# Optimization experiments

Hardware: AMD Instinct MI355X
Metric: run time of the kernel (lower is better)

## Reference

```python
import jax, jax.numpy as jnp
import numpy as np

NUM_USERS = 100000
NUM_ITEMS = 50000
N_NODES = NUM_USERS + NUM_ITEMS
N_EDGES = 2400000
EMB = 64
BATCH = 4096
GCN_LAYERS = 3
TAU = 0.2
SSL_LAMBDA = 0.1
REG_LAMBDA = 1e-4


def setup_inputs() -> dict:
    key = jax.random.key(0)
    ks = jax.random.split(key, 8)
    user = jax.random.randint(ks[0], (BATCH,), 0, NUM_USERS, dtype=jnp.int32)
    pos_item = jax.random.randint(ks[1], (BATCH,), 0, NUM_ITEMS, dtype=jnp.int32)
    neg_item = jax.random.randint(ks[2], (BATCH,), 0, NUM_ITEMS, dtype=jnp.int32)
    # symmetric bipartite edges: user -> item and item -> user
    half = N_EDGES // 2
    src_u = jax.random.randint(ks[3], (half,), 0, NUM_USERS, dtype=jnp.int32)
    dst_i = jax.random.randint(ks[4], (half,), NUM_USERS, N_NODES, dtype=jnp.int32)
    adj_row = jnp.concatenate([src_u, dst_i])
    adj_col = jnp.concatenate([dst_i, src_u])
    # normalized-adjacency-like small positive values
    adj_val = jax.random.uniform(ks[5], (N_EDGES,), dtype=jnp.float32) * 0.01
    user_emb_w = jax.random.normal(ks[6], (NUM_USERS, EMB), dtype=jnp.float32) * 0.1
    item_emb_w = jax.random.normal(ks[7], (NUM_ITEMS, EMB), dtype=jnp.float32) * 0.1
    return {"user": user, "pos_item": pos_item, "neg_item": neg_item,
            "adj_row": adj_row, "adj_col": adj_col, "adj_val": adj_val,
            "user_emb_w": user_emb_w, "item_emb_w": item_emb_w}


def _aggregate(adj_row, adj_col, adj_val, user_emb_w, item_emb_w):
    emb = jnp.concatenate([user_emb_w, item_emb_w], axis=0)  # [N, d]
    acc = emb
    e = emb
    for _ in range(GCN_LAYERS):
        # sparse.mm(adj, e): gather columns, scale, scatter-add into rows
        e = jax.ops.segment_sum(adj_val[:, None] * e[adj_col], adj_row,
                                num_segments=N_NODES)
        acc = acc + e
    final = acc / (GCN_LAYERS + 1)  # mean over stacked layer outputs
    return final[:NUM_USERS], final[NUM_USERS:]


def reference(user, pos_item, neg_item, adj_row, adj_col, adj_val,
              user_emb_w, item_emb_w):
    user_all, item_all = _aggregate(adj_row, adj_col, adj_val,
                                    user_emb_w, item_emb_w)
    u = user_all[user]          # [B, d]
    pos = item_all[pos_item]    # [B, d]
    neg = item_all[neg_item]    # [B, d]
    # BPR loss
    pos_s = jnp.sum(u * pos, axis=-1)
    neg_s = jnp.sum(u * neg, axis=-1)
    bpr_loss = -jnp.mean(jax.nn.log_sigmoid(pos_s - neg_s))
    # L2 regularization
    b = u.shape[0]
    reg_loss = 0.5 * (jnp.sum(u * u) + jnp.sum(pos * pos) + jnp.sum(neg * neg)) / b
    reg_loss = reg_loss * REG_LAMBDA
    # neighbor-aggregate SSL (InfoNCE between user and its positive item)
    un = u / jnp.linalg.norm(u, axis=-1, keepdims=True)
    pn = pos / jnp.linalg.norm(pos, axis=-1, keepdims=True)
    logits = un @ pn.T / TAU                       # [B, B]
    pos_logit = jnp.diagonal(logits)
    na_loss = jnp.mean(jax.nn.logsumexp(logits, axis=1) - pos_logit) * SSL_LAMBDA
    return bpr_loss + reg_loss + na_loss
```

## Files before the change

kernel.cpp:

```cpp
#include <hip/hip_runtime.h>
#include <hip/hip_fp16.h>
#include <math.h>

#define NUM_USERS 100000
#define NUM_ITEMS 50000
#define N_NODES   150000
#define N_EDGES   2400000
#define HALF_E    (N_EDGES / 2)
#define EMB       64
#define BATCH     4096
#define TAU        0.2f
#define SSL_LAMBDA 0.1f
#define REG_LAMBDA 1e-4f

#define NB        293
#define BROWS     512
#define CAP       13632
#define BINA_BLK  1024
#define CAST_BLK  9375

__device__ __forceinline__ float wave_sum(float v) {
    #pragma unroll
    for (int m = 1; m < 64; m <<= 1) v += __shfl_xor(v, m, 64);
    return v;
}
__device__ __forceinline__ __half2 bits2h2(int b) {
    union { int i; __half2 h; } u; u.i = b; return u.h;
}
__device__ __forceinline__ int h22bits(__half2 h) {
    union { int i; __half2 h; } u; u.h = h; return u.i;
}
__device__ __forceinline__ float h2f(unsigned short s) {
    union { unsigned short s; __half h; } u; u.s = s; return __half2float(u.h);
}

__global__ __launch_bounds__(256) void prep_kernel(
        const float4* __restrict__ uw4, const float4* __restrict__ iw4,
        uint2* __restrict__ h,
        const int* __restrict__ row, const int* __restrict__ col,
        const float* __restrict__ val,
        int* __restrict__ bucket_cursor, int2* __restrict__ arena) {
    __shared__ int hist[NB];
    const int t = threadIdx.x;
    size_t i = (size_t)blockIdx.x * 256 + t;
    const size_t tot = (size_t)N_NODES * EMB / 4;
    if (i < tot) {
        const size_t nu = (size_t)NUM_USERS * EMB / 4;
        float4 v = (i < nu) ? uw4[i] : iw4[i - nu];
        h[i] = make_uint2(h22bits(__floats2half2_rn(v.x, v.y)),
                          h22bits(__floats2half2_rn(v.z, v.w)));
    }
    if (blockIdx.x >= BINA_BLK) return;
    for (int k = t; k < NB; k += 256) hist[k] = 0;
    __syncthreads();
    const int per = (HALF_E + BINA_BLK - 1) / BINA_BLK;
    const int beg = blockIdx.x * per;
    const int end = min(beg + per, HALF_E);
    for (int e = beg + t; e < end; e += 256) {
        int r = row[e], c = col[e];
        atomicAdd(&hist[r >> 9], 1);
        atomicAdd(&hist[c >> 9], 1);
    }
    __syncthreads();
    for (int k = t; k < NB; k += 256) {
        int cnt = hist[k];
        int base = cnt ? atomicAdd(&bucket_cursor[k], cnt) : 0;
        hist[k] = k * CAP + base;
    }
    __syncthreads();
    for (int e = beg + t; e < end; e += 256) {
        int r = row[e], c = col[e];
        float v1 = val[e], v2 = val[e + HALF_E];
        int s1 = atomicAdd(&hist[r >> 9], 1);
        int s2 = atomicAdd(&hist[c >> 9], 1);
        arena[s1] = make_int2(c | ((r & 511) << 18), __float_as_int(v1));
        arena[s2] = make_int2(r | ((c & 511) << 18), __float_as_int(v2));
    }
}

__global__ __launch_bounds__(256) void bucket_scan(
        const int* __restrict__ bucket_cursor, int* __restrict__ bucket_base,
        int* __restrict__ rowptr) {
    __shared__ int sm[256];
    const int t = threadIdx.x;
    const int K = (NB + 255) / 256;
    int v[K], s = 0;
    #pragma unroll
    for (int j = 0; j < K; j++) {
        int idx = t * K + j;
        v[j] = (idx < NB) ? bucket_cursor[idx] : 0;
        s += v[j];
    }
    sm[t] = s;
    __syncthreads();
    for (int m = 1; m < 256; m <<= 1) {
        int y = (t >= m) ? sm[t - m] : 0;
        __syncthreads();
        sm[t] += y;
        __syncthreads();
    }
    int excl = sm[t] - s;
    #pragma unroll
    for (int j = 0; j < K; j++) {
        int idx = t * K + j;
        if (idx < NB) bucket_base[idx] = excl;
        excl += v[j];
    }
    if (t == 0) rowptr[N_NODES] = N_EDGES;
}

__global__ __launch_bounds__(1024) void bin_sort(
        const int* __restrict__ bucket_cursor, const int* __restrict__ bucket_base,
        const int2* __restrict__ arena,
        int* __restrict__ rowptr, int2* __restrict__ colval) {
    __shared__ int rcnt[BROWS];
    __shared__ int sm[256];
    const int bin = blockIdx.x;
    const int t = threadIdx.x;
    const int total = bucket_cursor[bin];
    const int count = min(total, CAP);
    const int gbase = bucket_base[bin];
    if (t < BROWS) rcnt[t] = 0;
    __syncthreads();
    for (int i = t; i < count; i += 1024) {
        int rx = arena[bin * CAP + i].x >> 18;
        atomicAdd(&rcnt[rx], 1);
    }
    __syncthreads();
    int v0 = 0, v1 = 0, s = 0;
    if (t < 256) {
        v0 = rcnt[2 * t]; v1 = rcnt[2 * t + 1];
        s = v0 + v1;
        sm[t] = s;
    }
    __syncthreads();
    for (int m = 1; m < 256; m <<= 1) {
        int y = (t < 256 && t >= m) ? sm[t - m] : 0;
        __syncthreads();
        if (t < 256) sm[t] += y;
        __syncthreads();
    }
    if (t < 256) {
        int excl = sm[t] - s;
        rcnt[2 * t] = excl;
        rcnt[2 * t + 1] = excl + v0;
        int r0 = bin * BROWS + 2 * t;
        if (r0 < N_NODES) rowptr[r0] = gbase + excl;
        if (r0 + 1 < N_NODES) rowptr[r0 + 1] = gbase + excl + v0;
    }
    __syncthreads();
    for (int i = t; i < count; i += 1024) {
        int2 rec = arena[bin * CAP + i];
        int pos = atomicAdd(&rcnt[rec.x >> 18], 1);
        __half2 hv = __float2half2_rn(__int_as_float(rec.y));
        colval[gbase + pos] = make_int2(rec.x & 0x3FFFF, h22bits(hv));
    }
    for (int i = count + t; i < total; i += 1024)
        colval[gbase + i] = make_int2(0, 0);
}

__global__ __launch_bounds__(256) void spmm_csr(
        const int* __restrict__ rowptr, const int2* __restrict__ colval,
        const unsigned short* __restrict__ h_cur, unsigned short* __restrict__ h_next) {
    const int t = threadIdx.x;
    const int lane = t & 63;
    const int g = lane >> 3;
    const int l = lane & 7;
    int r = blockIdx.x * 4 + (t >> 6);
    if (r >= N_NODES) return;
    const int beg = rowptr[r], end = rowptr[r + 1];
    __half2 ac0 = __float2half2_rn(0.0f), ac1 = ac0, ac2 = ac0, ac3 = ac0;
    int e = beg + g;
    if (e < end) {
        int2 cv = colval[e];
        uint4 x = ((const uint4*)(h_cur + (size_t)cv.x * EMB))[l];
        e += 8;
        if (e < end) {
            int2 cv2 = colval[e];
            uint4 x2 = ((const uint4*)(h_cur + (size_t)cv2.x * EMB))[l];
            for (e += 8; e < end; e += 8) {
                int2 cv3 = colval[e];
                uint4 x3 = ((const uint4*)(h_cur + (size_t)cv3.x * EMB))[l];
                __half2 vv = bits2h2(cv.y);
                ac0 = __hfma2(vv, bits2h2(x.x), ac0);
                ac1 = __hfma2(vv, bits2h2(x.y), ac1);
                ac2 = __hfma2(vv, bits2h2(x.z), ac2);
                ac3 = __hfma2(vv, bits2h2(x.w), ac3);
                cv = cv2; x = x2; cv2 = cv3; x2 = x3;
            }
            __half2 vv = bits2h2(cv.y);
            ac0 = __hfma2(vv, bits2h2(x.x), ac0);
            ac1 = __hfma2(vv, bits2h2(x.y), ac1);
            ac2 = __hfma2(vv, bits2h2(x.z), ac2);
            ac3 = __hfma2(vv, bits2h2(x.w), ac3);
            cv = cv2; x = x2;
        }
        __half2 vv = bits2h2(cv.y);
        ac0 = __hfma2(vv, bits2h2(x.x), ac0);
        ac1 = __hfma2(vv, bits2h2(x.y), ac1);
        ac2 = __hfma2(vv, bits2h2(x.z), ac2);
        ac3 = __hfma2(vv, bits2h2(x.w), ac3);
    }
    int a0 = h22bits(ac0), a1 = h22bits(ac1), a2 = h22bits(ac2), a3 = h22bits(ac3);
    #pragma unroll
    for (int m = 8; m < 64; m <<= 1) {
        a0 = h22bits(__hadd2(bits2h2(a0), bits2h2(__shfl_xor(a0, m, 64))));
        a1 = h22bits(__hadd2(bits2h2(a1), bits2h2(__shfl_xor(a1, m, 64))));
        a2 = h22bits(__hadd2(bits2h2(a2), bits2h2(__shfl_xor(a2, m, 64))));
        a3 = h22bits(__hadd2(bits2h2(a3), bits2h2(__shfl_xor(a3, m, 64))));
    }
    if (g == 0)
        ((uint4*)(h_next + (size_t)r * EMB))[l] =
            make_uint4((unsigned)a0, (unsigned)a1, (unsigned)a2, (unsigned)a3);
}

__global__ __launch_bounds__(256) void spmm_sel(
        const int* __restrict__ rowptr, const int2* __restrict__ colval,
        const int* __restrict__ user, const int* __restrict__ pos,
        const int* __restrict__ neg,
        const unsigned short* __restrict__ h_cur, float* __restrict__ sel) {
    const int t = threadIdx.x;
    const int lane = t & 63;
    const int g = lane >> 3;
    const int l = lane & 7;
    int b = blockIdx.x * 4 + (t >> 6);
    if (b >= 3 * BATCH) return;
    int which = b / BATCH, bb = b - which * BATCH;
    int r = (which == 0) ? user[bb]
          : NUM_USERS + ((which == 1) ? pos[bb] : neg[bb]);
    const int beg = rowptr[r], end = rowptr[r + 1];
    __half2 ac0 = __float2half2_rn(0.0f), ac1 = ac0, ac2 = ac0, ac3 = ac0;
    int e = beg + g;
    if (e < end) {
        int2 cv = colval[e];
        uint4 x = ((const uint4*)(h_cur + (size_t)cv.x * EMB))[l];
        e += 8;
        if (e < end) {
            int2 cv2 = colval[e];
            uint4 x2 = ((const uint4*)(h_cur + (size_t)cv2.x * EMB))[l];
            for (e += 8; e < end; e += 8) {
                int2 cv3 = colval[e];
                uint4 x3 = ((const uint4*)(h_cur + (size_t)cv3.x * EMB))[l];
                __half2 vv = bits2h2(cv.y);
                ac0 = __hfma2(vv, bits2h2(x.x), ac0);
                ac1 = __hfma2(vv, bits2h2(x.y), ac1);
                ac2 = __hfma2(vv, bits2h2(x.z), ac2);
                ac3 = __hfma2(vv, bits2h2(x.w), ac3);
                cv = cv2; x = x2; cv2 = cv3; x2 = x3;
            }
            __half2 vv = bits2h2(cv.y);
            ac0 = __hfma2(vv, bits2h2(x.x), ac0);
            ac1 = __hfma2(vv, bits2h2(x.y), ac1);
            ac2 = __hfma2(vv, bits2h2(x.z), ac2);
            ac3 = __hfma2(vv, bits2h2(x.w), ac3);
            cv = cv2; x = x2;
        }
        __half2 vv = bits2h2(cv.y);
        ac0 = __hfma2(vv, bits2h2(x.x), ac0);
        ac1 = __hfma2(vv, bits2h2(x.y), ac1);
        ac2 = __hfma2(vv, bits2h2(x.z), ac2);
        ac3 = __hfma2(vv, bits2h2(x.w), ac3);
    }
    int a0 = h22bits(ac0), a1 = h22bits(ac1), a2 = h22bits(ac2), a3 = h22bits(ac3);
    #pragma unroll
    for (int m = 8; m < 64; m <<= 1) {
        a0 = h22bits(__hadd2(bits2h2(a0), bits2h2(__shfl_xor(a0, m, 64))));
        a1 = h22bits(__hadd2(bits2h2(a1), bits2h2(__shfl_xor(a1, m, 64))));
        a2 = h22bits(__hadd2(bits2h2(a2), bits2h2(__shfl_xor(a2, m, 64))));
        a3 = h22bits(__hadd2(bits2h2(a3), bits2h2(__shfl_xor(a3, m, 64))));
    }
    if (g == 0) {
        float2 f0 = __half22float2(bits2h2(a0));
        float2 f1 = __half22float2(bits2h2(a1));
        float2 f2 = __half22float2(bits2h2(a2));
        float2 f3 = __half22float2(bits2h2(a3));
        uint4 hx = ((const uint4*)(h_cur + (size_t)r * EMB))[l];
        float2 s0 = __half22float2(bits2h2((int)hx.x));
        float2 s1 = __half22float2(bits2h2((int)hx.y));
        float2 s2 = __half22float2(bits2h2((int)hx.z));
        float2 s3 = __half22float2(bits2h2((int)hx.w));
        float4* dst = (float4*)(sel + (size_t)b * EMB);
        dst[2 * l]     = make_float4(f0.x + s0.x, f0.y + s0.y, f1.x + s1.x, f1.y + s1.y);
        dst[2 * l + 1] = make_float4(f2.x + s2.x, f2.y + s2.y, f3.x + s3.x, f3.y + s3.y);
    }
}

__global__ __launch_bounds__(256) void batch_loss(
        const int* __restrict__ user, const int* __restrict__ pos,
        const int* __restrict__ neg,
        const float* __restrict__ uw, const float* __restrict__ iw,
        const unsigned short* __restrict__ h1,
        const float* __restrict__ sel,
        float* __restrict__ un, float* __restrict__ pn,
        float* __restrict__ diag,
        float* __restrict__ pbpr, float* __restrict__ preg) {
    __shared__ float lb[4], lr[4];
    const int t = threadIdx.x;
    const int lane = t & 63;
    const int w = t >> 6;
    int b = blockIdx.x * 4 + w;
    const float inv4 = 0.25f;
    int nu = user[b], np = pos[b], ng = neg[b];
    float u = (uw[(size_t)nu * EMB + lane]
             + h2f(h1[(size_t)nu * EMB + lane])
             + sel[(size_t)b * EMB + lane]) * inv4;
    float p = (iw[(size_t)np * EMB + lane]
             + h2f(h1[(size_t)(NUM_USERS + np) * EMB + lane])
             + sel[(size_t)(BATCH + b) * EMB + lane]) * inv4;
    float n = (iw[(size_t)ng * EMB + lane]
             + h2f(h1[(size_t)(NUM_USERS + ng) * EMB + lane])
             + sel[(size_t)(2 * BATCH + b) * EMB + lane]) * inv4;
    float pos_s = wave_sum(u * p);
    float neg_s = wave_sum(u * n);
    float uu = wave_sum(u * u);
    float pp = wave_sum(p * p);
    float nn = wave_sum(n * n);
    float ru = rsqrtf(uu), rp = rsqrtf(pp);
    un[(size_t)b * EMB + lane] = u * ru;
    pn[(size_t)b * EMB + lane] = p * rp;
    if (lane == 0) {
        diag[b] = pos_s * ru * rp * (1.0f / TAU);
        float d = pos_s - neg_s;
        float tt = -d;
        lb[w] = fmaxf(tt, 0.0f) + log1pf(expf(-fabsf(tt)));
        lr[w] = uu + pp + nn;
    }
    __syncthreads();
    if (t == 0) {
        pbpr[blockIdx.x] = lb[0] + lb[1] + lb[2] + lb[3];
        preg[blockIdx.x] = lr[0] + lr[1] + lr[2] + lr[3];
    }
}

#define TS 128
__global__ __launch_bounds__(256) void ssl_gemm(
        const float* __restrict__ un, const float* __restrict__ pn,
        float* __restrict__ rowsum_p) {
    __shared__ float ua[EMB][TS];
    __shared__ float pb[EMB][TS];
    const int t = threadIdx.x;
    const int it = blockIdx.x & 31, jt = blockIdx.x >> 5;
    const int i0 = it * TS;
    const int j0 = jt * TS;
    for (int x = t; x < TS * 16; x += 256) {
        int i = x & (TS - 1), d4 = x >> 7;
        float4 v = ((const float4*)(un + (size_t)(i0 + i) * EMB))[d4];
        ua[d4 * 4 + 0][i] = v.x; ua[d4 * 4 + 1][i] = v.y;
        ua[d4 * 4 + 2][i] = v.z; ua[d4 * 4 + 3][i] = v.w;
        float4 w = ((const float4*)(pn + (size_t)(j0 + i) * EMB))[d4];
        pb[d4 * 4 + 0][i] = w.x; pb[d4 * 4 + 1][i] = w.y;
        pb[d4 * 4 + 2][i] = w.z; pb[d4 * 4 + 3][i] = w.w;
    }
    __syncthreads();
    const int tx = t & 15, ty = t >> 4;
    float c[8][8];
    #pragma unroll
    for (int p = 0; p < 8; p++)
        #pragma unroll
        for (int q = 0; q < 8; q++) c[p][q] = 0.0f;
    for (int k = 0; k < EMB; k++) {
        float a[8], b[8];
        #pragma unroll
        for (int q = 0; q < 8; q++) { a[q] = ua[k][ty * 8 + q]; b[q] = pb[k][tx * 8 + q]; }
        #pragma unroll
        for (int p = 0; p < 8; p++)
            #pragma unroll
            for (int q = 0; q < 8; q++) c[p][q] = fmaf(a[p], b[q], c[p][q]);
    }
    float s[8];
    #pragma unroll
    for (int p = 0; p < 8; p++) {
        s[p] = 0.0f;
        #pragma unroll
        for (int q = 0; q < 8; q++) s[p] += __expf(c[p][q] * (1.0f / TAU));
    }
    #pragma unroll
    for (int m = 1; m < 16; m <<= 1)
        #pragma unroll
        for (int p = 0; p < 8; p++) s[p] += __shfl_xor(s[p], m, 64);
    if (tx == 0) {
        #pragma unroll
        for (int p = 0; p < 8; p++)
            rowsum_p[(size_t)jt * BATCH + i0 + ty * 8 + p] = s[p];
    }
}

__global__ __launch_bounds__(256) void finalize(
        const float* __restrict__ rowsum_p, const float* __restrict__ diag,
        const float* __restrict__ pbpr, const float* __restrict__ preg,
        float* __restrict__ out) {
    __shared__ float red[3][4];
    const int t = threadIdx.x;
    float sb = 0.0f, sr = 0.0f, ss = 0.0f;
    for (int i = t; i < BATCH / 4; i += 256) { sb += pbpr[i]; sr += preg[i]; }
    for (int i = t; i < BATCH; i += 256) {
        float rs = 0.0f;
        #pragma unroll
        for (int j = 0; j < 32; j++) rs += rowsum_p[(size_t)j * BATCH + i];
        ss += logf(rs) - diag[i];
    }
    sb = wave_sum(sb); sr = wave_sum(sr); ss = wave_sum(ss);
    const int w = t >> 6;
    if ((t & 63) == 0) { red[0][w] = sb; red[1][w] = sr; red[2][w] = ss; }
    __syncthreads();
    if (t == 0) {
        float bpr_sum = red[0][0] + red[0][1] + red[0][2] + red[0][3];
        float reg_sum = red[1][0] + red[1][1] + red[1][2] + red[1][3];
        float ssl_sum = red[2][0] + red[2][1] + red[2][2] + red[2][3];
        float bpr = bpr_sum * (1.0f / BATCH);
        float reg = 0.5f * reg_sum * (1.0f / BATCH) * REG_LAMBDA;
        float ssl = ssl_sum * (1.0f / BATCH) * SSL_LAMBDA;
        out[0] = bpr + reg + ssl;
    }
}

extern "C" void kernel_launch(void* const* d_in, const int* in_sizes, int n_in,
                              void* d_out, int out_size, void* d_ws, size_t ws_size,
                              hipStream_t stream) {
    const int*   user    = (const int*)d_in[0];
    const int*   pos     = (const int*)d_in[1];
    const int*   neg     = (const int*)d_in[2];
    const int*   adj_row = (const int*)d_in[3];
    const int*   adj_col = (const int*)d_in[4];
    const float* adj_val = (const float*)d_in[5];
    const float* user_w  = (const float*)d_in[6];
    const float* item_w  = (const float*)d_in[7];
    float* out = (float*)d_out;

    unsigned short* hA = (unsigned short*)d_ws;
    unsigned short* hB = hA + (size_t)N_NODES * EMB;
    float* buf1   = (float*)d_ws + (size_t)N_NODES * EMB;
    float* sel    = buf1 + (size_t)N_NODES * EMB;
    float* un     = sel  + (size_t)3 * BATCH * EMB;
    float* pn     = un   + (size_t)BATCH * EMB;
    float* diag   = pn   + (size_t)BATCH * EMB;
    float* rowsum_p = diag + BATCH;
    float* pbpr   = rowsum_p + 32 * BATCH;
    float* preg   = pbpr + 1024;
    int*   rowptr = (int*)(preg + 1024);
    int*   bucket_cursor = rowptr + 150016;
    int*   bucket_base   = bucket_cursor + 512;
    int2*  colval = (int2*)(bucket_base + 512);
    int2*  arena  = (int2*)buf1;

    hipMemsetAsync(bucket_cursor, 0, 512 * sizeof(int), stream);

    dim3 blk(256);

    prep_kernel<<<CAST_BLK, blk, 0, stream>>>((const float4*)user_w,
                                              (const float4*)item_w, (uint2*)hA,
                                              adj_row, adj_col, adj_val,
                                              bucket_cursor, arena);
    bucket_scan<<<1, blk, 0, stream>>>(bucket_cursor, bucket_base, rowptr);
    bin_sort<<<NB, dim3(1024), 0, stream>>>(bucket_cursor, bucket_base, arena,
                                            rowptr, colval);

    spmm_csr<<<(N_NODES + 3) / 4, blk, 0, stream>>>(rowptr, colval, hA, hB);
    spmm_csr<<<(N_NODES + 3) / 4, blk, 0, stream>>>(rowptr, colval, hB, hA);
    spmm_sel<<<(3 * BATCH + 3) / 4, blk, 0, stream>>>(rowptr, colval, user, pos,
                                                      neg, hA, sel);

    batch_loss<<<BATCH / 4, blk, 0, stream>>>(user, pos, neg, user_w, item_w,
                                              hB, sel, un, pn, diag, pbpr, preg);
    ssl_gemm<<<(BATCH / TS) * (BATCH / TS), blk, 0, stream>>>(un, pn, rowsum_p);
    finalize<<<1, blk, 0, stream>>>(rowsum_p, diag, pbpr, preg, out);
}
```

Baseline: 349.0 us.

## Stage binned edges in shared memory for coalesced bucket writes

New measurement: 317.5 us. 9.0% less time.

```diff
diff --git a/kernel.cpp b/kernel.cpp
--- a/kernel.cpp
+++ b/kernel.cpp
@@ -16,7 +16,9 @@
 #define NB        293
 #define BROWS     512
 #define CAP       13632
-#define BINA_BLK  1024
+#define BINA_BLK  512
+#define PER_BLK   ((HALF_E + BINA_BLK - 1) / BINA_BLK)
+#define EBUF_CAP  (2 * PER_BLK)
 #define CAST_BLK  9375
 
 __device__ __forceinline__ float wave_sum(float v) {
@@ -32,6 +34,9 @@
 }
 __device__ __forceinline__ float h2f(unsigned short s) {
     union { unsigned short s; __half h; } u; u.s = s; return __half2float(u.h);
+}
+__device__ __forceinline__ unsigned short f2h_bits(float x) {
+    union { __half h; unsigned short s; } u; u.h = __float2half_rn(x); return u.s;
 }
 
 __global__ __launch_bounds__(256) void prep_kernel(
@@ -41,6 +46,10 @@
         const float* __restrict__ val,
         int* __restrict__ bucket_cursor, int2* __restrict__ arena) {
     __shared__ int hist[NB];
+    __shared__ int lbase[NB];
+    __shared__ int delta[NB];
+    __shared__ int sm[256];
+    __shared__ int2 ebuf[EBUF_CAP];
     const int t = threadIdx.x;
     size_t i = (size_t)blockIdx.x * 256 + t;
     const size_t tot = (size_t)N_NODES * EMB / 4;
@@ -53,28 +62,53 @@
     if (blockIdx.x >= BINA_BLK) return;
     for (int k = t; k < NB; k += 256) hist[k] = 0;
     __syncthreads();
-    const int per = (HALF_E + BINA_BLK - 1) / BINA_BLK;
-    const int beg = blockIdx.x * per;
-    const int end = min(beg + per, HALF_E);
+    const int beg = blockIdx.x * PER_BLK;
+    const int end = min(beg + PER_BLK, HALF_E);
     for (int e = beg + t; e < end; e += 256) {
         int r = row[e], c = col[e];
         atomicAdd(&hist[r >> 9], 1);
         atomicAdd(&hist[c >> 9], 1);
     }
     __syncthreads();
+    int v0 = (2 * t < NB) ? hist[2 * t] : 0;
+    int v1 = (2 * t + 1 < NB) ? hist[2 * t + 1] : 0;
+    int s = v0 + v1;
+    sm[t] = s;
+    __syncthreads();
+    for (int m = 1; m < 256; m <<= 1) {
+        int y = (t >= m) ? sm[t - m] : 0;
+        __syncthreads();
+        sm[t] += y;
+        __syncthreads();
+    }
+    int excl = sm[t] - s;
+    if (2 * t < NB) lbase[2 * t] = excl;
+    if (2 * t + 1 < NB) lbase[2 * t + 1] = excl + v0;
+    __syncthreads();
     for (int k = t; k < NB; k += 256) {
         int cnt = hist[k];
-        int base = cnt ? atomicAdd(&bucket_cursor[k], cnt) : 0;
-        hist[k] = k * CAP + base;
-    }
+        int gb = cnt ? atomicAdd(&bucket_cursor[k], cnt) : 0;
+        delta[k] = (k * CAP + gb) - lbase[k];
+    }
+    __syncthreads();
+    for (int k = t; k < NB; k += 256) hist[k] = lbase[k];
     __syncthreads();
     for (int e = beg + t; e < end; e += 256) {
         int r = row[e], c = col[e];
-        float v1 = val[e], v2 = val[e + HALF_E];
-        int s1 = atomicAdd(&hist[r >> 9], 1);
-        int s2 = atomicAdd(&hist[c >> 9], 1);
-        arena[s1] = make_int2(c | ((r & 511) << 18), __float_as_int(v1));
-        arena[s2] = make_int2(r | ((c & 511) << 18), __float_as_int(v2));
+        unsigned short h1 = f2h_bits(val[e]);
+        unsigned short h2v = f2h_bits(val[e + HALF_E]);
+        int b1 = r >> 9, b2 = c >> 9;
+        int p1 = atomicAdd(&hist[b1], 1);
+        int p2 = atomicAdd(&hist[b2], 1);
+        ebuf[p1] = make_int2(c | ((r & 511) << 18), (b1 << 16) | h1);
+        ebuf[p2] = make_int2(r | ((c & 511) << 18), (b2 << 16) | h2v);
+    }
+    __syncthreads();
+    const int count = 2 * (end - beg);
+    for (int k = t; k < count; k += 256) {
+        int2 rec = ebuf[k];
+        int b = rec.y >> 16;
+        arena[k + delta[b]] = rec;
     }
 }
 
@@ -124,7 +158,7 @@
     __syncthreads();
     for (int i = t; i < count; i += 1024) {
         int rx = arena[bin * CAP + i].x >> 18;
-        atomicAdd(&rcnt[rx], 1);
+        atomicAdd(&rcnt[rx & 511], 1);
     }
     __syncthreads();
     int v0 = 0, v1 = 0, s = 0;
@@ -151,9 +185,9 @@
     __syncthreads();
     for (int i = t; i < count; i += 1024) {
         int2 rec = arena[bin * CAP + i];
-        int pos = atomicAdd(&rcnt[rec.x >> 18], 1);
-        __half2 hv = __float2half2_rn(__int_as_float(rec.y));
-        colval[gbase + pos] = make_int2(rec.x & 0x3FFFF, h22bits(hv));
+        int pos = atomicAdd(&rcnt[(rec.x >> 18) & 511], 1);
+        unsigned int hv = (unsigned int)rec.y & 0xFFFFu;
+        colval[gbase + pos] = make_int2(rec.x & 0x3FFFF, (int)(hv * 0x10001u));
     }
     for (int i = count + t; i < total; i += 1024)
         colval[gbase + i] = make_int2(0, 0);
```
